# Kernel optimization log

Measured on AMD Instinct MI355X. Metric: run time of the kernel, lower is better.

## Reference

```python
import jax, jax.numpy as jnp
import numpy as np

E = 1024
FF = 4096
EPS = 1e-5


def _linear(x, W, b):
    # x: [B,S,in], W: [in,out], b: [out]
    return jnp.einsum('bsi,io->bso', x, W) + b


def _layernorm(x, g, b):
    mu = jnp.mean(x, axis=-1, keepdims=True)
    var = jnp.mean(jnp.square(x - mu), axis=-1, keepdims=True)
    return (x - mu) * jax.lax.rsqrt(var + EPS) * g + b


def setup_inputs() -> dict:
    key = jax.random.key(0)
    ks = jax.random.split(key, 8)
    s = 0.02
    inp = {
        'src': jax.random.normal(ks[0], (4, 2048, E), dtype=jnp.float32),
        'Wq': jax.random.normal(ks[1], (E, E), dtype=jnp.float32) * s,
        'bq': jnp.zeros((E,), jnp.float32),
        'Wk': jax.random.normal(ks[2], (E, E), dtype=jnp.float32) * s,
        'bk': jnp.zeros((E,), jnp.float32),
        'Wv': jax.random.normal(ks[3], (E, E), dtype=jnp.float32) * s,
        'bv': jnp.zeros((E,), jnp.float32),
        'Wo': jax.random.normal(ks[4], (E, E), dtype=jnp.float32) * s,
        'bo': jnp.zeros((E,), jnp.float32),
        'W1': jax.random.normal(ks[5], (E, FF), dtype=jnp.float32) * s,
        'b1': jnp.zeros((FF,), jnp.float32),
        'W2': jax.random.normal(ks[6], (FF, E), dtype=jnp.float32) * s,
        'b2': jnp.zeros((E,), jnp.float32),
        'g1': jnp.ones((E,), jnp.float32),
        'be1': jnp.zeros((E,), jnp.float32),
        'g2': jnp.ones((E,), jnp.float32),
        'be2': jnp.zeros((E,), jnp.float32),
    }
    return inp


def reference(src, Wq, bq, Wk, bk, Wv, bv, Wo, bo, W1, b1, W2, b2, g1, be1, g2, be2):
    Q = _linear(src, Wq, bq)
    K = _linear(src, Wk, bk)
    V = _linear(src, Wv, bv)
    # Single-head attention, NO 1/sqrt(d) scaling (faithful to source)
    scores = jnp.einsum('bqe,bke->bqk', Q, K)  # [B,S,S]
    weights = jax.nn.softmax(scores, axis=-1)
    attn = jnp.einsum('bqk,bke->bqe', weights, V)
    attn = _linear(attn, Wo, bo)
    x = _layernorm(src + attn, g1, be1)
    ff = _linear(x, W1, b1)
    ff = jax.nn.relu(ff)
    ff = _linear(ff, W2, b2)
    return _layernorm(x + ff, g2, be2)
```

## Files before the change

### kernel.cpp

```cpp
#include <hip/hip_runtime.h>
#include <hip/hip_bf16.h>


using u16 = unsigned short;
typedef __attribute__((ext_vector_type(8))) _Float16 half8;
typedef __attribute__((ext_vector_type(4))) float f32x4;

#define BATCH 4
#define SEQ   2048
#define EMB   1024
#define FFD   4096

#define SWZ(r) ((((r) >> 1) & 3) << 4)

__device__ __forceinline__ u16 f2h(float f) {
    union { _Float16 h; u16 u; } x;
    x.h = (_Float16)f;
    return x.u;
}

typedef const __attribute__((address_space(1))) void* gas_ptr;
typedef __attribute__((address_space(3))) void* las_ptr;

__device__ __forceinline__ void load_lds16(const void* g, void* l) {
    __builtin_amdgcn_global_load_lds((gas_ptr)g, (las_ptr)l, 16, 0, 0);
}

#define VM8 asm volatile("s_waitcnt vmcnt(8)" ::: "memory")
#define VM6 asm volatile("s_waitcnt vmcnt(6)" ::: "memory")
#define VM4 asm volatile("s_waitcnt vmcnt(4)" ::: "memory")
#define VM3 asm volatile("s_waitcnt vmcnt(3)" ::: "memory")
#define VM0 asm volatile("s_waitcnt vmcnt(0)" ::: "memory")
#define VMNONE ((void)0)

template <int BM, typename OutT, bool RELU, bool BIAS>
__global__ __launch_bounds__(512, 2) void gemm_dp(
    const u16* __restrict__ A, const u16* __restrict__ Bt,
    OutT* __restrict__ C, const float* __restrict__ bias,
    int N, int K, int lda, int ldb, int ldc, long sA, long sB, long sC)
{
    constexpr int MF = BM / 32;
    constexpr int AL = BM / 128;
    constexpr int AH = BM * 32;
    constexpr int BH = 256 * 32;

    __shared__ u16 ldsA[4 * AH];
    __shared__ u16 ldsB[4 * BH];

    A  += (long)blockIdx.z * sA;
    Bt += (long)blockIdx.z * sB;
    C  += (long)blockIdx.z * sC;

    const int tid  = threadIdx.x;
    const int lane = tid & 63;
    const int wv   = tid >> 6;
    const int wm   = wv >> 2;
    const int wn   = wv & 3;
    const long row0 = (long)blockIdx.x * BM;
    const long col0 = (long)blockIdx.y * 256;

    long aoff[AL]; int adst[AL];
#pragma unroll
    for (int i = 0; i < AL; ++i) {
        const int d16 = i * 512 + tid;
        const int row = d16 >> 2;
        const int colb = ((d16 & 3) << 4) ^ SWZ(row);
        aoff[i] = (row0 + row) * (long)lda + (colb >> 1);
        adst[i] = d16 * 16;
    }
    long boff[2]; int bdst[2];
#pragma unroll
    for (int i = 0; i < 2; ++i) {
        const int d16 = i * 512 + tid;
        const int row = d16 >> 2;
        const int colb = ((d16 & 3) << 4) ^ SWZ(row);
        boff[i] = (col0 + row) * (long)ldb + (colb >> 1);
        bdst[i] = d16 * 16;
    }

    int aro[MF], bro[4];
    const int klane = (lane >> 4) << 4;
#pragma unroll
    for (int m = 0; m < MF; ++m) {
        const int row = wm * (BM / 2) + m * 16 + (lane & 15);
        aro[m] = row * 64 + (klane ^ SWZ(row));
    }
#pragma unroll
    for (int n = 0; n < 4; ++n) {
        const int row = wn * 64 + n * 16 + (lane & 15);
        bro[n] = row * 64 + (klane ^ SWZ(row));
    }

    f32x4 acc[MF][4] = {};
    const int G = K >> 5;

    auto stage = [&](int g) {
        const int slot = g & 3;
        const long k0 = (long)g << 5;
#pragma unroll
        for (int i = 0; i < AL; ++i)
            load_lds16(A + aoff[i] + k0, (char*)ldsA + slot * (AH * 2) + adst[i]);
#pragma unroll
        for (int i = 0; i < 2; ++i)
            load_lds16(Bt + boff[i] + k0, (char*)ldsB + slot * (BH * 2) + bdst[i]);
    };

#define GBODY(g, VMASM, DOSTAGE)                                              \
    {                                                                         \
        const int slot_ = (g) & 3;                                            \
        const char* abase_ = (const char*)ldsA + slot_ * (AH * 2);            \
        const char* bbase_ = (const char*)ldsB + slot_ * (BH * 2);            \
        half8 a_[MF], b_[4];                                                  \
        _Pragma("unroll") for (int m = 0; m < MF; ++m)                        \
            a_[m] = *(const half8*)(abase_ + aro[m]);                         \
        _Pragma("unroll") for (int n = 0; n < 4; ++n)                         \
            b_[n] = *(const half8*)(bbase_ + bro[n]);                         \
        if (DOSTAGE) stage((g) + 3);                                          \
        VMASM;                                                                \
        __builtin_amdgcn_s_setprio(1);                                        \
        _Pragma("unroll") for (int m = 0; m < MF; ++m)                        \
            _Pragma("unroll") for (int n = 0; n < 4; ++n)                     \
                acc[m][n] = __builtin_amdgcn_mfma_f32_16x16x32_f16(           \
                    a_[m], b_[n], acc[m][n], 0, 0, 0);                        \
        __builtin_amdgcn_s_setprio(0);                                        \
        __builtin_amdgcn_s_barrier();                                         \
        __builtin_amdgcn_sched_barrier(0);                                    \
    }

    stage(0); stage(1); stage(2);
    if constexpr (BM == 256) { VM8; } else { VM6; }
    __builtin_amdgcn_s_barrier();
    __builtin_amdgcn_sched_barrier(0);

    for (int g = 0; g < G - 3; ++g) {
        if constexpr (BM == 256) GBODY(g, VM8, true)
        else                     GBODY(g, VM6, true)
    }
    if constexpr (BM == 256) { GBODY(G - 3, VM4, false) }
    else                     { GBODY(G - 3, VM3, false) }
    GBODY(G - 2, VM0, false)
    GBODY(G - 1, VMNONE, false)
#undef GBODY

#pragma unroll
    for (int n = 0; n < 4; ++n) {
        const long col = col0 + wn * 64 + n * 16 + (lane & 15);
        const float bv_ = BIAS ? bias[col] : 0.0f;
#pragma unroll
        for (int m = 0; m < MF; ++m) {
            const long row = row0 + wm * (BM / 2) + m * 16 + ((lane >> 4) << 2);
#pragma unroll
            for (int r = 0; r < 4; ++r) {
                float v = acc[m][n][r] + bv_;
                if (RELU) v = fmaxf(v, 0.0f);
                if constexpr (sizeof(OutT) == 2)
                    C[(row + r) * (long)ldc + col] = f2h(v);
                else
                    C[(row + r) * (long)ldc + col] = v;
            }
        }
    }
}

__global__ __launch_bounds__(256) void transpose_cast(
    const float* __restrict__ in, u16* __restrict__ out, int R, int C)
{
    __shared__ float t[32][33];
    const int bc = blockIdx.x * 32, br = blockIdx.y * 32;
    const int lx = threadIdx.x & 31, ly = threadIdx.x >> 5;
#pragma unroll
    for (int i = 0; i < 32; i += 8)
        t[ly + i][lx] = in[(long)(br + ly + i) * C + bc + lx];
    __syncthreads();
#pragma unroll
    for (int i = 0; i < 32; i += 8)
        out[(long)(bc + ly + i) * R + br + lx] = f2h(t[lx][ly + i]);
}

__global__ __launch_bounds__(256) void transpose_h(
    const u16* __restrict__ in, u16* __restrict__ out,
    int ldin, int ldout, long sIn, long sOut)
{
    __shared__ u16 t[32][33];
    in  += (long)blockIdx.z * sIn;
    out += (long)blockIdx.z * sOut;
    const int bc = blockIdx.x * 32, br = blockIdx.y * 32;
    const int lx = threadIdx.x & 31, ly = threadIdx.x >> 5;
#pragma unroll
    for (int i = 0; i < 32; i += 8)
        t[ly + i][lx] = in[(long)(br + ly + i) * ldin + bc + lx];
    __syncthreads();
#pragma unroll
    for (int i = 0; i < 32; i += 8)
        out[(long)(bc + ly + i) * ldout + br + lx] = t[lx][ly + i];
}

__global__ __launch_bounds__(256) void cast_h(
    const float* __restrict__ in, u16* __restrict__ out)
{
    const long i = ((long)blockIdx.x * 256 + threadIdx.x) * 8;
    const float4 a = ((const float4*)(in + i))[0];
    const float4 b = ((const float4*)(in + i))[1];
    union { u16 u[8]; uint4 v; } pk;
    pk.u[0] = f2h(a.x); pk.u[1] = f2h(a.y); pk.u[2] = f2h(a.z); pk.u[3] = f2h(a.w);
    pk.u[4] = f2h(b.x); pk.u[5] = f2h(b.y); pk.u[6] = f2h(b.z); pk.u[7] = f2h(b.w);
    *(uint4*)(out + i) = pk.v;
}

__global__ __launch_bounds__(256) void concat_bias(
    const float* __restrict__ bq, const float* __restrict__ bk,
    const float* __restrict__ bv, float* __restrict__ o)
{
    const int i = blockIdx.x * 256 + threadIdx.x;
    o[i] = i < 1024 ? bq[i] : (i < 2048 ? bk[i - 1024] : bv[i - 2048]);
}

__global__ __launch_bounds__(256) void softmax_kernel(
    const float* __restrict__ S, u16* __restrict__ P)
{
    const long row = blockIdx.x;
    const float* src = S + row * SEQ;
    const int tid = threadIdx.x;

    const float4 v0 = ((const float4*)src)[tid * 2];
    const float4 v1 = ((const float4*)src)[tid * 2 + 1];

    float m = fmaxf(fmaxf(fmaxf(v0.x, v0.y), fmaxf(v0.z, v0.w)),
                    fmaxf(fmaxf(v1.x, v1.y), fmaxf(v1.z, v1.w)));
#pragma unroll
    for (int off = 32; off; off >>= 1) m = fmaxf(m, __shfl_xor(m, off));

    __shared__ float rm[4], rs[4];
    if ((tid & 63) == 0) rm[tid >> 6] = m;
    __syncthreads();
    m = fmaxf(fmaxf(rm[0], rm[1]), fmaxf(rm[2], rm[3]));

    float e[8];
    e[0] = expf(v0.x - m); e[1] = expf(v0.y - m);
    e[2] = expf(v0.z - m); e[3] = expf(v0.w - m);
    e[4] = expf(v1.x - m); e[5] = expf(v1.y - m);
    e[6] = expf(v1.z - m); e[7] = expf(v1.w - m);

    float s = ((e[0] + e[1]) + (e[2] + e[3])) + ((e[4] + e[5]) + (e[6] + e[7]));
#pragma unroll
    for (int off = 32; off; off >>= 1) s += __shfl_xor(s, off);
    if ((tid & 63) == 0) rs[tid >> 6] = s;
    __syncthreads();
    s = (rs[0] + rs[1]) + (rs[2] + rs[3]);

    const float inv = 1.0f / s;
    union { u16 u[8]; uint4 v; } pk;
#pragma unroll
    for (int j = 0; j < 8; ++j) pk.u[j] = f2h(e[j] * inv);
    *(uint4*)(P + row * SEQ + tid * 8) = pk.v;
}

__global__ __launch_bounds__(256) void ln_kernel(
    const float* __restrict__ Ain, const float* __restrict__ Bin,
    const float* __restrict__ g, const float* __restrict__ be,
    float* __restrict__ Xout, u16* __restrict__ Xh)
{
    const long row = blockIdx.x;
    const int tid = threadIdx.x;

    const float4 a = ((const float4*)(Ain + row * EMB))[tid];
    const float4 b = ((const float4*)(Bin + row * EMB))[tid];
    const float h0 = a.x + b.x, h1 = a.y + b.y, h2 = a.z + b.z, h3 = a.w + b.w;

    float s = (h0 + h1) + (h2 + h3);
    float q = (h0 * h0 + h1 * h1) + (h2 * h2 + h3 * h3);
#pragma unroll
    for (int off = 32; off; off >>= 1) {
        s += __shfl_xor(s, off);
        q += __shfl_xor(q, off);
    }
    __shared__ float rsm[4], rqm[4];
    if ((tid & 63) == 0) { rsm[tid >> 6] = s; rqm[tid >> 6] = q; }
    __syncthreads();
    s = (rsm[0] + rsm[1]) + (rsm[2] + rsm[3]);
    q = (rqm[0] + rqm[1]) + (rqm[2] + rqm[3]);

    const float mu  = s * (1.0f / EMB);
    const float var = q * (1.0f / EMB) - mu * mu;
    const float rstd = rsqrtf(var + 1e-5f);

    const float4 gv = ((const float4*)g)[tid];
    const float4 bv = ((const float4*)be)[tid];
    const float y0 = (h0 - mu) * rstd * gv.x + bv.x;
    const float y1 = (h1 - mu) * rstd * gv.y + bv.y;
    const float y2 = (h2 - mu) * rstd * gv.z + bv.z;
    const float y3 = (h3 - mu) * rstd * gv.w + bv.w;

    ((float4*)(Xout + row * EMB))[tid] = make_float4(y0, y1, y2, y3);
    if (Xh) {
        union { u16 u[4]; uint2 v; } pk;
        pk.u[0] = f2h(y0); pk.u[1] = f2h(y1);
        pk.u[2] = f2h(y2); pk.u[3] = f2h(y3);
        ((uint2*)(Xh + row * EMB))[tid] = pk.v;
    }
}

extern "C" void kernel_launch(void* const* d_in, const int* in_sizes, int n_in,
                              void* d_out, int out_size, void* d_ws, size_t ws_size,
                              hipStream_t stream)
{
    const float* src = (const float*)d_in[0];
    const float* Wq  = (const float*)d_in[1];
    const float* bq  = (const float*)d_in[2];
    const float* Wk  = (const float*)d_in[3];
    const float* bk  = (const float*)d_in[4];
    const float* Wv  = (const float*)d_in[5];
    const float* bv  = (const float*)d_in[6];
    const float* Wo  = (const float*)d_in[7];
    const float* bo  = (const float*)d_in[8];
    const float* W1  = (const float*)d_in[9];
    const float* b1  = (const float*)d_in[10];
    const float* W2  = (const float*)d_in[11];
    const float* b2  = (const float*)d_in[12];
    const float* g1  = (const float*)d_in[13];
    const float* be1 = (const float*)d_in[14];
    const float* g2  = (const float*)d_in[15];
    const float* be2 = (const float*)d_in[16];
    float* out = (float*)d_out;

    char* ws = (char*)d_ws;
    const size_t MB = 1ull << 20;
    u16*   WqkvT = (u16*)  (ws + 0 * MB);
    u16*   WoT   = (u16*)  (ws + 6 * MB);
    u16*   W1T   = (u16*)  (ws + 8 * MB);
    u16*   W2T   = (u16*)  (ws + 16 * MB);
    float* bqkv  = (float*)(ws + 24 * MB);
    u16*   Xh    = (u16*)  (ws + 25 * MB);
    u16*   QKVh  = (u16*)  (ws + 41 * MB);
    u16*   Vt    = (u16*)  (ws + 89 * MB);
    float* scores= (float*)(ws + 105 * MB);
    u16*   P     = (u16*)  (ws + 169 * MB);
    u16*   attn  = (u16*)  (ws + 105 * MB);
    float* attnp = (float*)(ws + 121 * MB);
    u16*   xh    = (u16*)  (ws + 41 * MB);
    float* x     = (float*)(ws + 169 * MB);
    u16*   ff1   = (u16*)  (ws + 105 * MB);
    float* ff2   = (float*)(ws + 57 * MB);

    const int M = BATCH * SEQ;
    const long SS = (long)SEQ * SEQ;

    transpose_cast<<<dim3(32, 32, 1), 256, 0, stream>>>(Wq, WqkvT, EMB, EMB);
    transpose_cast<<<dim3(32, 32, 1), 256, 0, stream>>>(Wk, WqkvT + 1024 * 1024, EMB, EMB);
    transpose_cast<<<dim3(32, 32, 1), 256, 0, stream>>>(Wv, WqkvT + 2048 * 1024, EMB, EMB);
    transpose_cast<<<dim3(32, 32, 1), 256, 0, stream>>>(Wo, WoT, EMB, EMB);
    transpose_cast<<<dim3(128, 32, 1), 256, 0, stream>>>(W1, W1T, EMB, FFD);
    transpose_cast<<<dim3(32, 128, 1), 256, 0, stream>>>(W2, W2T, FFD, EMB);
    concat_bias<<<dim3(12), 256, 0, stream>>>(bq, bk, bv, bqkv);

    cast_h<<<dim3((M * EMB) / (256 * 8)), 256, 0, stream>>>(src, Xh);

    gemm_dp<256, u16, false, true><<<dim3(32, 12, 1), 512, 0, stream>>>(
        Xh, WqkvT, QKVh, bqkv, 3072, 1024, 1024, 1024, 3072, 0, 0, 0);

    transpose_h<<<dim3(32, 64, BATCH), 256, 0, stream>>>(
        QKVh + 2048, Vt, 3072, SEQ, (long)SEQ * 3072, (long)EMB * SEQ);

    gemm_dp<256, float, false, false><<<dim3(8, 8, BATCH), 512, 0, stream>>>(
        QKVh, QKVh + 1024, scores, nullptr, SEQ, EMB, 3072, 3072, SEQ,
        (long)SEQ * 3072, (long)SEQ * 3072, SS);

    softmax_kernel<<<dim3(M), 256, 0, stream>>>(scores, P);

    gemm_dp<128, u16, false, false><<<dim3(16, 4, BATCH), 512, 0, stream>>>(
        P, Vt, attn, nullptr, EMB, SEQ, SEQ, SEQ, EMB,
        SS, (long)EMB * SEQ, (long)SEQ * EMB);

    gemm_dp<128, float, false, true><<<dim3(64, 4, 1), 512, 0, stream>>>(
        attn, WoT, attnp, bo, EMB, EMB, EMB, EMB, EMB, 0, 0, 0);

    ln_kernel<<<dim3(M), 256, 0, stream>>>(src, attnp, g1, be1, x, xh);

    gemm_dp<256, u16, true, true><<<dim3(32, 16, 1), 512, 0, stream>>>(
        xh, W1T, ff1, b1, FFD, EMB, EMB, EMB, FFD, 0, 0, 0);

    gemm_dp<128, float, false, true><<<dim3(64, 4, 1), 512, 0, stream>>>(
        ff1, W2T, ff2, b2, EMB, FFD, FFD, FFD, EMB, 0, 0, 0);

    ln_kernel<<<dim3(M), 256, 0, stream>>>(x, ff2, g2, be2, out, nullptr);
}
```

Before: 434.2 us.

## Double-buffer LDS fragment reads in GEMM and store attention scores in fp16

Restructures the GEMM inner loop to split A fragments into two halves with ping-pong register buffers, prefetching the next LDS fragments while MFMAs on the current half execute. It also makes the QK^T GEMM emit fp16 scores and the softmax read fp16, halving scores memory traffic. The extra barriers per K-step add synchronisation cost. Rounding unscaled logits to fp16 reduces softmax accuracy and risks overflow for large scores.

```diff
diff --git a/kernel.cpp b/kernel.cpp
--- a/kernel.cpp
+++ b/kernel.cpp
@@ -18,6 +18,11 @@
     x.h = (_Float16)f;
     return x.u;
 }
+__device__ __forceinline__ float h2f(u16 u) {
+    union { u16 u; _Float16 h; } x;
+    x.u = u;
+    return (float)x.h;
+}
 
 typedef const __attribute__((address_space(1))) void* gas_ptr;
 typedef __attribute__((address_space(3))) void* las_ptr;
@@ -25,13 +30,6 @@
 __device__ __forceinline__ void load_lds16(const void* g, void* l) {
     __builtin_amdgcn_global_load_lds((gas_ptr)g, (las_ptr)l, 16, 0, 0);
 }
-
-#define VM8 asm volatile("s_waitcnt vmcnt(8)" ::: "memory")
-#define VM6 asm volatile("s_waitcnt vmcnt(6)" ::: "memory")
-#define VM4 asm volatile("s_waitcnt vmcnt(4)" ::: "memory")
-#define VM3 asm volatile("s_waitcnt vmcnt(3)" ::: "memory")
-#define VM0 asm volatile("s_waitcnt vmcnt(0)" ::: "memory")
-#define VMNONE ((void)0)
 
 template <int BM, typename OutT, bool RELU, bool BIAS>
 __global__ __launch_bounds__(512, 2) void gemm_dp(
@@ -40,12 +38,13 @@
     int N, int K, int lda, int ldb, int ldc, long sA, long sB, long sC)
 {
     constexpr int MF = BM / 32;
+    constexpr int MH = MF / 2;
     constexpr int AL = BM / 128;
-    constexpr int AH = BM * 32;
-    constexpr int BH = 256 * 32;
-
-    __shared__ u16 ldsA[4 * AH];
-    __shared__ u16 ldsB[4 * BH];
+    constexpr int SLAB_A = BM * 32;
+    constexpr int SLAB_B = 256 * 32;
+
+    __shared__ u16 ldsA[4 * SLAB_A];
+    __shared__ u16 ldsB[4 * SLAB_B];
 
     A  += (long)blockIdx.z * sA;
     Bt += (long)blockIdx.z * sB;
@@ -78,20 +77,14 @@
         bdst[i] = d16 * 16;
     }
 
-    int aro[MF], bro[4];
     const int klane = (lane >> 4) << 4;
-#pragma unroll
-    for (int m = 0; m < MF; ++m) {
-        const int row = wm * (BM / 2) + m * 16 + (lane & 15);
-        aro[m] = row * 64 + (klane ^ SWZ(row));
-    }
-#pragma unroll
-    for (int n = 0; n < 4; ++n) {
-        const int row = wn * 64 + n * 16 + (lane & 15);
-        bro[n] = row * 64 + (klane ^ SWZ(row));
-    }
+    const int arow = wm * (BM / 2) + (lane & 15);
+    const int aro0 = arow * 64 + (klane ^ SWZ(arow));
+    const int brow = wn * 64 + (lane & 15);
+    const int bro0 = brow * 64 + (klane ^ SWZ(brow));
 
     f32x4 acc[MF][4] = {};
+    half8 Aa[MH], Ab[MH], Ba[4], Bb[4];
     const int G = K >> 5;
 
     auto stage = [&](int g) {
@@ -99,48 +92,57 @@
         const long k0 = (long)g << 5;
 #pragma unroll
         for (int i = 0; i < AL; ++i)
-            load_lds16(A + aoff[i] + k0, (char*)ldsA + slot * (AH * 2) + adst[i]);
+            load_lds16(A + aoff[i] + k0, (char*)ldsA + slot * (SLAB_A * 2) + adst[i]);
 #pragma unroll
         for (int i = 0; i < 2; ++i)
-            load_lds16(Bt + boff[i] + k0, (char*)ldsB + slot * (BH * 2) + bdst[i]);
+            load_lds16(Bt + boff[i] + k0, (char*)ldsB + slot * (SLAB_B * 2) + bdst[i]);
     };
 
-#define GBODY(g, VMASM, DOSTAGE)                                              \
+#define LDSA_P(slot) ((const char*)ldsA + (slot) * (SLAB_A * 2))
+#define LDSB_P(slot) ((const char*)ldsB + (slot) * (SLAB_B * 2))
+#define RD_A(dst, slot, mh)                                                   \
+    _Pragma("unroll") for (int i_ = 0; i_ < MH; ++i_)                         \
+        dst[i_] = *(const half8*)(LDSA_P(slot) + aro0 + ((mh) * MH + i_) * 1024);
+#define RD_B(dst, slot)                                                       \
+    _Pragma("unroll") for (int n_ = 0; n_ < 4; ++n_)                          \
+        dst[n_] = *(const half8*)(LDSB_P(slot) + bro0 + n_ * 1024);
+#define MM(Ax, Bx, mh)                                                        \
+    __builtin_amdgcn_s_setprio(1);                                            \
+    _Pragma("unroll") for (int i_ = 0; i_ < MH; ++i_)                         \
+    _Pragma("unroll") for (int n_ = 0; n_ < 4; ++n_)                          \
+        acc[(mh) * MH + i_][n_] = __builtin_amdgcn_mfma_f32_16x16x32_f16(     \
+            Ax[i_], Bx[n_], acc[(mh) * MH + i_][n_], 0, 0, 0);                \
+    __builtin_amdgcn_s_setprio(0);
+#define BAR { __builtin_amdgcn_s_barrier(); __builtin_amdgcn_sched_barrier(0); }
+#define VMS  { if constexpr (BM == 256) asm volatile("s_waitcnt vmcnt(8)" ::: "memory"); \
+               else                     asm volatile("s_waitcnt vmcnt(6)" ::: "memory"); }
+#define VMT  { if constexpr (BM == 256) asm volatile("s_waitcnt vmcnt(4)" ::: "memory"); \
+               else                     asm volatile("s_waitcnt vmcnt(3)" ::: "memory"); }
+#define VM0  asm volatile("s_waitcnt vmcnt(0)" ::: "memory")
+
+    stage(0); stage(1); stage(2);
+    VMS; BAR;
+    RD_A(Aa, 0, 0); RD_B(Ba, 0);
+
+#define PAIR(S, DOSTG0, VMA, DOSTG1, VMB)                                     \
     {                                                                         \
-        const int slot_ = (g) & 3;                                            \
-        const char* abase_ = (const char*)ldsA + slot_ * (AH * 2);            \
-        const char* bbase_ = (const char*)ldsB + slot_ * (BH * 2);            \
-        half8 a_[MF], b_[4];                                                  \
-        _Pragma("unroll") for (int m = 0; m < MF; ++m)                        \
-            a_[m] = *(const half8*)(abase_ + aro[m]);                         \
-        _Pragma("unroll") for (int n = 0; n < 4; ++n)                         \
-            b_[n] = *(const half8*)(bbase_ + bro[n]);                         \
-        if (DOSTAGE) stage((g) + 3);                                          \
-        VMASM;                                                                \
-        __builtin_amdgcn_s_setprio(1);                                        \
-        _Pragma("unroll") for (int m = 0; m < MF; ++m)                        \
-            _Pragma("unroll") for (int n = 0; n < 4; ++n)                     \
-                acc[m][n] = __builtin_amdgcn_mfma_f32_16x16x32_f16(           \
-                    a_[m], b_[n], acc[m][n], 0, 0, 0);                        \
-        __builtin_amdgcn_s_setprio(0);                                        \
-        __builtin_amdgcn_s_barrier();                                         \
-        __builtin_amdgcn_sched_barrier(0);                                    \
-    }
-
-    stage(0); stage(1); stage(2);
-    if constexpr (BM == 256) { VM8; } else { VM6; }
-    __builtin_amdgcn_s_barrier();
-    __builtin_amdgcn_sched_barrier(0);
-
-    for (int g = 0; g < G - 3; ++g) {
-        if constexpr (BM == 256) GBODY(g, VM8, true)
-        else                     GBODY(g, VM6, true)
-    }
-    if constexpr (BM == 256) { GBODY(G - 3, VM4, false) }
-    else                     { GBODY(G - 3, VM3, false) }
-    GBODY(G - 2, VM0, false)
-    GBODY(G - 1, VMNONE, false)
-#undef GBODY
+        if (DOSTG0) stage((S) + 3);                                           \
+        RD_A(Ab, (S) & 3, 1); VMA; MM(Aa, Ba, 0); BAR;                        \
+        RD_A(Aa, ((S) + 1) & 3, 0); RD_B(Bb, ((S) + 1) & 3);                  \
+        MM(Ab, Ba, 1); BAR;                                                   \
+        if (DOSTG1) stage((S) + 4);                                           \
+        RD_A(Ab, ((S) + 1) & 3, 1); VMB; MM(Aa, Bb, 0); BAR;                  \
+        RD_A(Aa, ((S) + 2) & 3, 0); RD_B(Ba, ((S) + 2) & 3);                  \
+        MM(Ab, Bb, 1); BAR;                                                   \
+    }
+
+    for (int s = 0; s <= G - 6; s += 2) PAIR(s, true, VMS, true, VMS)
+    PAIR(G - 4, true, VMS, false, VMT)
+    RD_A(Ab, (G - 2) & 3, 1); VM0; MM(Aa, Ba, 0); BAR;
+    RD_A(Aa, (G - 1) & 3, 0); RD_B(Bb, (G - 1) & 3); MM(Ab, Ba, 1); BAR;
+    RD_A(Ab, (G - 1) & 3, 1); MM(Aa, Bb, 0); BAR;
+    MM(Ab, Bb, 1);
+#undef PAIR
 
 #pragma unroll
     for (int n = 0; n < 4; ++n) {
@@ -160,6 +162,15 @@
             }
         }
     }
+#undef LDSA_P
+#undef LDSB_P
+#undef RD_A
+#undef RD_B
+#undef MM
+#undef BAR
+#undef VMS
+#undef VMT
+#undef VM0
 }
 
 __global__ __launch_bounds__(256) void transpose_cast(
@@ -216,17 +227,19 @@
 }
 
 __global__ __launch_bounds__(256) void softmax_kernel(
-    const float* __restrict__ S, u16* __restrict__ P)
+    const u16* __restrict__ S, u16* __restrict__ P)
 {
     const long row = blockIdx.x;
-    const float* src = S + row * SEQ;
     const int tid = threadIdx.x;
 
-    const float4 v0 = ((const float4*)src)[tid * 2];
-    const float4 v1 = ((const float4*)src)[tid * 2 + 1];
-
-    float m = fmaxf(fmaxf(fmaxf(v0.x, v0.y), fmaxf(v0.z, v0.w)),
-                    fmaxf(fmaxf(v1.x, v1.y), fmaxf(v1.z, v1.w)));
+    union { uint4 v; u16 u[8]; } in;
+    in.v = ((const uint4*)(S + row * SEQ))[tid];
+    float f[8];
+#pragma unroll
+    for (int j = 0; j < 8; ++j) f[j] = h2f(in.u[j]);
+
+    float m = fmaxf(fmaxf(fmaxf(f[0], f[1]), fmaxf(f[2], f[3])),
+                    fmaxf(fmaxf(f[4], f[5]), fmaxf(f[6], f[7])));
 #pragma unroll
     for (int off = 32; off; off >>= 1) m = fmaxf(m, __shfl_xor(m, off));
 
@@ -235,13 +248,9 @@
     __syncthreads();
     m = fmaxf(fmaxf(rm[0], rm[1]), fmaxf(rm[2], rm[3]));
 
-    float e[8];
-    e[0] = expf(v0.x - m); e[1] = expf(v0.y - m);
-    e[2] = expf(v0.z - m); e[3] = expf(v0.w - m);
-    e[4] = expf(v1.x - m); e[5] = expf(v1.y - m);
-    e[6] = expf(v1.z - m); e[7] = expf(v1.w - m);
-
-    float s = ((e[0] + e[1]) + (e[2] + e[3])) + ((e[4] + e[5]) + (e[6] + e[7]));
+    float e[8], s = 0.0f;
+#pragma unroll
+    for (int j = 0; j < 8; ++j) { e[j] = expf(f[j] - m); s += e[j]; }
 #pragma unroll
     for (int off = 32; off; off >>= 1) s += __shfl_xor(s, off);
     if ((tid & 63) == 0) rs[tid >> 6] = s;
@@ -325,22 +334,22 @@
 
     char* ws = (char*)d_ws;
     const size_t MB = 1ull << 20;
-    u16*   WqkvT = (u16*)  (ws + 0 * MB);
-    u16*   WoT   = (u16*)  (ws + 6 * MB);
-    u16*   W1T   = (u16*)  (ws + 8 * MB);
-    u16*   W2T   = (u16*)  (ws + 16 * MB);
-    float* bqkv  = (float*)(ws + 24 * MB);
-    u16*   Xh    = (u16*)  (ws + 25 * MB);
-    u16*   QKVh  = (u16*)  (ws + 41 * MB);
-    u16*   Vt    = (u16*)  (ws + 89 * MB);
-    float* scores= (float*)(ws + 105 * MB);
-    u16*   P     = (u16*)  (ws + 169 * MB);
-    u16*   attn  = (u16*)  (ws + 105 * MB);
-    float* attnp = (float*)(ws + 121 * MB);
-    u16*   xh    = (u16*)  (ws + 41 * MB);
-    float* x     = (float*)(ws + 169 * MB);
-    u16*   ff1   = (u16*)  (ws + 105 * MB);
-    float* ff2   = (float*)(ws + 57 * MB);
+    u16*   WqkvT   = (u16*)  (ws + 0 * MB);
+    u16*   WoT     = (u16*)  (ws + 6 * MB);
+    u16*   W1T     = (u16*)  (ws + 8 * MB);
+    u16*   W2T     = (u16*)  (ws + 16 * MB);
+    float* bqkv    = (float*)(ws + 24 * MB);
+    u16*   Xh      = (u16*)  (ws + 25 * MB);
+    u16*   QKVh    = (u16*)  (ws + 41 * MB);
+    u16*   Vt      = (u16*)  (ws + 89 * MB);
+    u16*   scoresh = (u16*)  (ws + 105 * MB);
+    u16*   P       = (u16*)  (ws + 137 * MB);
+    u16*   attn    = (u16*)  (ws + 105 * MB);
+    float* attnp   = (float*)(ws + 121 * MB);
+    float* x       = (float*)(ws + 153 * MB);
+    u16*   xh      = (u16*)  (ws + 41 * MB);
+    u16*   ff1     = (u16*)  (ws + 57 * MB);
+    float* ff2     = (float*)(ws + 121 * MB);
 
     const int M = BATCH * SEQ;
     const long SS = (long)SEQ * SEQ;
@@ -361,11 +370,11 @@
     transpose_h<<<dim3(32, 64, BATCH), 256, 0, stream>>>(
         QKVh + 2048, Vt, 3072, SEQ, (long)SEQ * 3072, (long)EMB * SEQ);
 
-    gemm_dp<256, float, false, false><<<dim3(8, 8, BATCH), 512, 0, stream>>>(
-        QKVh, QKVh + 1024, scores, nullptr, SEQ, EMB, 3072, 3072, SEQ,
+    gemm_dp<256, u16, false, false><<<dim3(8, 8, BATCH), 512, 0, stream>>>(
+        QKVh, QKVh + 1024, scoresh, nullptr, SEQ, EMB, 3072, 3072, SEQ,
         (long)SEQ * 3072, (long)SEQ * 3072, SS);
 
-    softmax_kernel<<<dim3(M), 256, 0, stream>>>(scores, P);
+    softmax_kernel<<<dim3(M), 256, 0, stream>>>(scoresh, P);
 
     gemm_dp<128, u16, false, false><<<dim3(16, 4, BATCH), 512, 0, stream>>>(
         P, Vt, attn, nullptr, EMB, SEQ, SEQ, SEQ, EMB,
```

New measurement: 515.1 us. +18.6%, slower.
